# Optimization experiments

Measured on AMD Instinct MI355X. Metric: run time of the kernel, lower is better.

## Reference

```python
import jax, jax.numpy as jnp
import numpy as np

DIM = 256
NUM_HEADS = 8
HEAD_DIM = DIM // NUM_HEADS          # 32
KEY_DIM = int(HEAD_DIM * 0.5)        # 16
SCALE = KEY_DIM ** (-0.5)
QKV_OUT = DIM + 2 * KEY_DIM * NUM_HEADS  # 512
BN_EPS = 1e-3


def _bn(x, gamma, beta, mean, var):
    # inference-mode BatchNorm2d over channel axis 1 of NCHW
    inv = gamma / jnp.sqrt(var + BN_EPS)
    return x * inv[None, :, None, None] + (beta - mean * inv)[None, :, None, None]


def _conv1x1(x, w):
    # w: (O, C, 1, 1)
    return jnp.einsum('bchw,oc->bohw', x, w[:, :, 0, 0])


def _dwconv3x3(x, w):
    # depthwise 3x3, SAME padding; w: (C, 1, 3, 3)
    return jax.lax.conv_general_dilated(
        x, w, window_strides=(1, 1), padding='SAME',
        feature_group_count=x.shape[1],
        dimension_numbers=('NCHW', 'OIHW', 'NCHW'))


def setup_inputs() -> dict:
    key = jax.random.key(0)
    ks = jax.random.split(key, 16)
    B, C, H, W = 16, DIM, 32, 32
    inp = {
        'x': jax.random.normal(ks[0], (B, C, H, W), jnp.float32),
        'qkv_w': jax.random.normal(ks[1], (QKV_OUT, DIM, 1, 1), jnp.float32) * (1.0 / np.sqrt(DIM)),
        'qkv_gamma': jnp.ones((QKV_OUT,), jnp.float32),
        'qkv_beta': jnp.zeros((QKV_OUT,), jnp.float32),
        'qkv_mean': jax.random.normal(ks[2], (QKV_OUT,), jnp.float32) * 0.1,
        'qkv_var': jax.random.uniform(ks[3], (QKV_OUT,), jnp.float32, 0.5, 1.5),
        'pe_w': jax.random.normal(ks[4], (DIM, 1, 3, 3), jnp.float32) * (1.0 / 3.0),
        'pe_gamma': jnp.ones((DIM,), jnp.float32),
        'pe_beta': jnp.zeros((DIM,), jnp.float32),
        'pe_mean': jax.random.normal(ks[5], (DIM,), jnp.float32) * 0.1,
        'pe_var': jax.random.uniform(ks[6], (DIM,), jnp.float32, 0.5, 1.5),
        'proj_w': jax.random.normal(ks[7], (DIM, DIM, 1, 1), jnp.float32) * (1.0 / np.sqrt(DIM)),
        'proj_gamma': jnp.ones((DIM,), jnp.float32),
        'proj_beta': jnp.zeros((DIM,), jnp.float32),
        'proj_mean': jax.random.normal(ks[8], (DIM,), jnp.float32) * 0.1,
        'proj_var': jax.random.uniform(ks[9], (DIM,), jnp.float32, 0.5, 1.5),
    }
    return inp


def reference(x, qkv_w, qkv_gamma, qkv_beta, qkv_mean, qkv_var,
              pe_w, pe_gamma, pe_beta, pe_mean, pe_var,
              proj_w, proj_gamma, proj_beta, proj_mean, proj_var):
    B, C, H, W = x.shape
    N = H * W
    # qkv: 1x1 conv + BN (act=False)
    qkv = _bn(_conv1x1(x, qkv_w), qkv_gamma, qkv_beta, qkv_mean, qkv_var)
    qkv = qkv.reshape(B, NUM_HEADS, 2 * KEY_DIM + HEAD_DIM, N)
    q = qkv[:, :, :KEY_DIM]                          # (B, h, kd, N)
    k = qkv[:, :, KEY_DIM:2 * KEY_DIM]               # (B, h, kd, N)
    v = qkv[:, :, 2 * KEY_DIM:]                      # (B, h, hd, N)
    # attn = (q^T @ k) * scale, softmax over last dim
    attn = jnp.einsum('bhdn,bhdm->bhnm', q, k) * SCALE   # (B, h, N, N)
    attn = jax.nn.softmax(attn, axis=-1)
    # v @ attn^T
    v_attn = jnp.einsum('bhdn,bhmn->bhdm', v, attn)      # (B, h, hd, N)
    v_attn = v_attn.reshape(B, C, H, W)
    v_reshaped = v.reshape(B, C, H, W)
    pos_enc = _bn(_dwconv3x3(v_reshaped, pe_w), pe_gamma, pe_beta, pe_mean, pe_var)
    out = v_attn + pos_enc
    out = _bn(_conv1x1(out, proj_w), proj_gamma, proj_beta, proj_mean, proj_var)
    return out
```

## Files before the change

### kernel.cpp

```cpp
#include <hip/hip_runtime.h>

#define B_ 16
#define C_ 256
#define N_ 1024
#define NH 8
#define HD 32
#define KD 16
#define QKV_OUT_ 512
#define BN_EPS 1e-3f
#define SCALE_ 0.25f

typedef __attribute__((ext_vector_type(8))) short short8;
typedef __attribute__((ext_vector_type(16))) float float16;

__device__ inline unsigned short f2bf(float f) {
  unsigned int u = __float_as_uint(f);
  return (unsigned short)((u + 0x7FFF + ((u >> 16) & 1)) >> 16);
}
__device__ inline float bf2f(unsigned short s) {
  return __uint_as_float(((unsigned int)s) << 16);
}
__device__ inline float16 zero16() {
  float16 z;
  #pragma unroll
  for (int i = 0; i < 16; ++i) z[i] = 0.f;
  return z;
}
__device__ inline unsigned int pack_bf16_trunc(float a, float b) {
  return __builtin_amdgcn_perm(__float_as_uint(b), __float_as_uint(a), 0x07060302u);
}

__global__ __launch_bounds__(256) void fold_weights(
    const float* __restrict__ qkv_w, const float* __restrict__ qg,
    const float* __restrict__ qb, const float* __restrict__ qm,
    const float* __restrict__ qv,
    const float* __restrict__ proj_w, const float* __restrict__ pg,
    const float* __restrict__ pb, const float* __restrict__ pm,
    const float* __restrict__ pv,
    unsigned short* __restrict__ wq, float* __restrict__ biasq,
    unsigned short* __restrict__ wp, float* __restrict__ biasp)
{
  const int o = blockIdx.x, c = threadIdx.x;
  if (o < QKV_OUT_) {
    float inv = qg[o] * rsqrtf(qv[o] + BN_EPS);
    wq[o * C_ + c] = f2bf(qkv_w[o * C_ + c] * inv);
    if (c == 0) biasq[o] = qb[o] - qm[o] * inv;
  } else {
    int oo = o - QKV_OUT_;
    float inv = pg[oo] * rsqrtf(pv[oo] + BN_EPS);
    wp[oo * C_ + c] = f2bf(proj_w[oo * C_ + c] * inv);
    if (c == 0) biasp[oo] = pb[oo] - pm[oo] * inv;
  }
}

template <int OC, bool BF16OUT>
__global__ __launch_bounds__(256) void gemm_bn(
    const float* __restrict__ in, const unsigned short* __restrict__ wfold,
    const float* __restrict__ bias, void* __restrict__ out)
{
  __shared__ __align__(16) unsigned short xb[128][24];
  const int tid = threadIdx.x;
  const int wave = tid >> 6, lane = tid & 63, l31 = lane & 31, lh = lane >> 5;
  const int wm = wave & 1, wn = wave >> 1;
  const int nt = blockIdx.x, ot = blockIdx.y, b = blockIdx.z;

  const float* inb = in + (size_t)b * C_ * N_ + nt * 128;
  const int srow = tid & 127, sc0 = (tid >> 7) * 8;

  float16 acc0 = zero16(), acc1 = zero16();
  const unsigned short* wrow = wfold + (size_t)(ot * 64 + wm * 32 + l31) * C_;

  for (int kc = 0; kc < C_; kc += 16) {
    float xv[8];
    #pragma unroll
    for (int j = 0; j < 8; ++j)
      xv[j] = inb[(size_t)(kc + sc0 + j) * N_ + srow];
    unsigned int pk[4];
    #pragma unroll
    for (int q = 0; q < 4; ++q) pk[q] = pack_bf16_trunc(xv[2*q], xv[2*q+1]);
    __syncthreads();
    *(uint4*)&xb[srow][sc0] = make_uint4(pk[0], pk[1], pk[2], pk[3]);
    __syncthreads();

    short8 af = *(const short8*)(wrow + kc + lh * 8);
    short8 b0 = *(const short8*)&xb[wn * 64 + l31][lh * 8];
    short8 b1 = *(const short8*)&xb[wn * 64 + 32 + l31][lh * 8];
    acc0 = __builtin_amdgcn_mfma_f32_32x32x16_bf16(af, b0, acc0, 0, 0, 0);
    acc1 = __builtin_amdgcn_mfma_f32_32x32x16_bf16(af, b1, acc1, 0, 0, 0);
  }

  #pragma unroll
  for (int r = 0; r < 16; ++r) {
    int o = ot * 64 + wm * 32 + (r & 3) + 8 * (r >> 2) + 4 * lh;
    float bo = bias[o];
    size_t base = ((size_t)b * OC + o) * N_ + nt * 128 + wn * 64 + l31;
    float v0 = acc0[r] + bo, v1 = acc1[r] + bo;
    if constexpr (BF16OUT) {
      ((unsigned short*)out)[base]      = f2bf(v0);
      ((unsigned short*)out)[base + 32] = f2bf(v1);
    } else {
      ((float*)out)[base]      = v0;
      ((float*)out)[base + 32] = v1;
    }
  }
}

__global__ __launch_bounds__(256) void attn_mfma(
    const unsigned short* __restrict__ qkvb, float* __restrict__ vattn)
{
  const int wave = threadIdx.x >> 6, lane = threadIdx.x & 63;
  const int l31 = lane & 31, lh = lane >> 5;
  const int h = blockIdx.y, b = blockIdx.z;
  const int qbase = blockIdx.x * 128 + wave * 32;

  const unsigned short* qp = qkvb + ((size_t)b * QKV_OUT_ + h * 64) * N_;
  const unsigned short* kp = qp + (size_t)KD * N_;
  const unsigned short* vp = qp + (size_t)(2 * KD) * N_;

  short8 qf;
  #pragma unroll
  for (int j = 0; j < 8; ++j)
    qf[j] = (short)f2bf(bf2f(qp[(size_t)(lh * 8 + j) * N_ + qbase + l31]) * SCALE_);

  float16 oacc = zero16();
  float lsum = 0.f;

  for (int kc = 0; kc < N_; kc += 128) {
    #pragma unroll
    for (int t = 0; t < 4; ++t) {
      short8 kf;
      #pragma unroll
      for (int j = 0; j < 8; ++j)
        kf[j] = (short)kp[(size_t)(lh * 8 + j) * N_ + kc + t * 32 + l31];
      float16 st = __builtin_amdgcn_mfma_f32_32x32x16_bf16(kf, qf, zero16(), 0, 0, 0);

      unsigned int u[8];
      #pragma unroll
      for (int q = 0; q < 8; ++q) {
        float pe = __expf(st[2 * q]);
        float po = __expf(st[2 * q + 1]);
        lsum += pe + po;
        u[q] = pack_bf16_trunc(pe, po);
      }
      unsigned int e[8];
      #pragma unroll
      for (int q = 0; q < 8; ++q)
        e[q] = (unsigned int)__shfl_xor((int)u[q], 32, 64);

      #pragma unroll
      for (int f = 0; f < 2; ++f) {
        union { unsigned int w[4]; short8 s; } bf;
        int q0 = f * 4;
        bf.w[0] = lh ? e[q0 + 2] : u[q0 + 0];
        bf.w[1] = lh ? e[q0 + 3] : u[q0 + 1];
        bf.w[2] = lh ? u[q0 + 2] : e[q0 + 0];
        bf.w[3] = lh ? u[q0 + 3] : e[q0 + 1];
        short8 vf = *(const short8*)(vp + (size_t)l31 * N_ + kc + t * 32 + f * 16 + lh * 8);
        oacc = __builtin_amdgcn_mfma_f32_32x32x16_bf16(vf, bf.s, oacc, 0, 0, 0);
      }
    }
  }

  lsum += __shfl_xor(lsum, 32, 64);
  float linv = 1.f / lsum;

  #pragma unroll
  for (int r = 0; r < 16; ++r) {
    int d = (r & 3) + 8 * (r >> 2) + 4 * lh;
    vattn[((size_t)b * C_ + h * HD + d) * N_ + qbase + l31] = oacc[r] * linv;
  }
}

__global__ __launch_bounds__(256) void dwconv_bn_add(
    const unsigned short* __restrict__ qkvb, const float* __restrict__ pw,
    const float* __restrict__ gamma, const float* __restrict__ beta,
    const float* __restrict__ mean, const float* __restrict__ var,
    float* __restrict__ vsum)
{
  __shared__ float t[34][34];
  const int c = blockIdx.x, b = blockIdx.y;
  const int tid = threadIdx.x;
  const int qc = (c >> 5) * 64 + 32 + (c & 31);
  const unsigned short* vp = qkvb + ((size_t)b * QKV_OUT_ + qc) * N_;

  #pragma unroll
  for (int r = 0; r < 4; ++r) {
    int idx = r * 256 + tid;
    t[(idx >> 5) + 1][(idx & 31) + 1] = bf2f(vp[idx]);
  }
  if (tid < 34) {
    t[0][tid] = 0.f; t[33][tid] = 0.f;
    t[tid][0] = 0.f; t[tid][33] = 0.f;
  }
  __syncthreads();

  float w9[9];
  #pragma unroll
  for (int i = 0; i < 9; ++i) w9[i] = pw[c * 9 + i];
  float inv = gamma[c] * rsqrtf(var[c] + BN_EPS);
  float add = beta[c] - mean[c] * inv;

  float* op = vsum + ((size_t)b * C_ + c) * N_;
  #pragma unroll
  for (int r = 0; r < 4; ++r) {
    int idx = r * 256 + tid;
    int y = idx >> 5, x = idx & 31;
    float s = 0.f;
    #pragma unroll
    for (int dy = 0; dy < 3; ++dy)
      #pragma unroll
      for (int dx = 0; dx < 3; ++dx)
        s += t[y + dy][x + dx] * w9[dy * 3 + dx];
    op[idx] = s * inv + add + op[idx];
  }
}

extern "C" void kernel_launch(void* const* d_in, const int* in_sizes, int n_in,
                              void* d_out, int out_size, void* d_ws, size_t ws_size,
                              hipStream_t stream) {
  const float* x          = (const float*)d_in[0];
  const float* qkv_w      = (const float*)d_in[1];
  const float* qkv_gamma  = (const float*)d_in[2];
  const float* qkv_beta   = (const float*)d_in[3];
  const float* qkv_mean   = (const float*)d_in[4];
  const float* qkv_var    = (const float*)d_in[5];
  const float* pe_w       = (const float*)d_in[6];
  const float* pe_gamma   = (const float*)d_in[7];
  const float* pe_beta    = (const float*)d_in[8];
  const float* pe_mean    = (const float*)d_in[9];
  const float* pe_var     = (const float*)d_in[10];
  const float* proj_w     = (const float*)d_in[11];
  const float* proj_gamma = (const float*)d_in[12];
  const float* proj_beta  = (const float*)d_in[13];
  const float* proj_mean  = (const float*)d_in[14];
  const float* proj_var   = (const float*)d_in[15];
  float* out = (float*)d_out;

  char* ws = (char*)d_ws;
  unsigned short* qkvb = (unsigned short*)ws;
  ws += (size_t)B_ * QKV_OUT_ * N_ * sizeof(unsigned short);
  float* vattn = (float*)ws;
  ws += (size_t)B_ * C_ * N_ * sizeof(float);
  unsigned short* wq = (unsigned short*)ws;
  ws += (size_t)QKV_OUT_ * C_ * sizeof(unsigned short);
  unsigned short* wp = (unsigned short*)ws;
  ws += (size_t)C_ * C_ * sizeof(unsigned short);
  float* biasq = (float*)ws; ws += QKV_OUT_ * sizeof(float);
  float* biasp = (float*)ws;

  fold_weights<<<dim3(QKV_OUT_ + C_), 256, 0, stream>>>(
      qkv_w, qkv_gamma, qkv_beta, qkv_mean, qkv_var,
      proj_w, proj_gamma, proj_beta, proj_mean, proj_var,
      wq, biasq, wp, biasp);

  gemm_bn<QKV_OUT_, true><<<dim3(8, 8, 16), 256, 0, stream>>>(x, wq, biasq, qkvb);

  attn_mfma<<<dim3(8, NH, B_), 256, 0, stream>>>(qkvb, vattn);

  dwconv_bn_add<<<dim3(C_, B_), 256, 0, stream>>>(
      qkvb, pe_w, pe_gamma, pe_beta, pe_mean, pe_var, vattn);

  gemm_bn<C_, false><<<dim3(8, 4, 16), 256, 0, stream>>>(vattn, wp, biasp, out);
}
```

Measured before the change: 179.0 us.

## Transpose Q/K to token-major layout, double-buffer GEMM tiles, use exp2 softmax

```diff
diff --git a/kernel.cpp b/kernel.cpp
--- a/kernel.cpp
+++ b/kernel.cpp
@@ -8,7 +8,7 @@
 #define KD 16
 #define QKV_OUT_ 512
 #define BN_EPS 1e-3f
-#define SCALE_ 0.25f
+#define SCALE2_ (0.25f * 1.44269504088896f)
 
 typedef __attribute__((ext_vector_type(8))) short short8;
 typedef __attribute__((ext_vector_type(16))) float float16;
@@ -53,74 +53,131 @@
   }
 }
 
-template <int OC, bool BF16OUT>
+template <int MODE>
 __global__ __launch_bounds__(256) void gemm_bn(
     const float* __restrict__ in, const unsigned short* __restrict__ wfold,
-    const float* __restrict__ bias, void* __restrict__ out)
+    const float* __restrict__ bias,
+    unsigned short* __restrict__ qkT, unsigned short* __restrict__ vbuf,
+    float* __restrict__ outf)
 {
-  __shared__ __align__(16) unsigned short xb[128][24];
+  __shared__ __align__(16) unsigned short xb[2][256][20];
   const int tid = threadIdx.x;
   const int wave = tid >> 6, lane = tid & 63, l31 = lane & 31, lh = lane >> 5;
   const int wm = wave & 1, wn = wave >> 1;
   const int nt = blockIdx.x, ot = blockIdx.y, b = blockIdx.z;
 
-  const float* inb = in + (size_t)b * C_ * N_ + nt * 128;
-  const int srow = tid & 127, sc0 = (tid >> 7) * 8;
-
-  float16 acc0 = zero16(), acc1 = zero16();
+  const float* inb = in + (size_t)b * C_ * N_ + nt * 256 + tid;
   const unsigned short* wrow = wfold + (size_t)(ot * 64 + wm * 32 + l31) * C_;
 
-  for (int kc = 0; kc < C_; kc += 16) {
-    float xv[8];
-    #pragma unroll
-    for (int j = 0; j < 8; ++j)
-      xv[j] = inb[(size_t)(kc + sc0 + j) * N_ + srow];
-    unsigned int pk[4];
-    #pragma unroll
-    for (int q = 0; q < 4; ++q) pk[q] = pack_bf16_trunc(xv[2*q], xv[2*q+1]);
-    __syncthreads();
-    *(uint4*)&xb[srow][sc0] = make_uint4(pk[0], pk[1], pk[2], pk[3]);
-    __syncthreads();
-
-    short8 af = *(const short8*)(wrow + kc + lh * 8);
-    short8 b0 = *(const short8*)&xb[wn * 64 + l31][lh * 8];
-    short8 b1 = *(const short8*)&xb[wn * 64 + 32 + l31][lh * 8];
-    acc0 = __builtin_amdgcn_mfma_f32_32x32x16_bf16(af, b0, acc0, 0, 0, 0);
-    acc1 = __builtin_amdgcn_mfma_f32_32x32x16_bf16(af, b1, acc1, 0, 0, 0);
-  }
-
-  #pragma unroll
-  for (int r = 0; r < 16; ++r) {
-    int o = ot * 64 + wm * 32 + (r & 3) + 8 * (r >> 2) + 4 * lh;
-    float bo = bias[o];
-    size_t base = ((size_t)b * OC + o) * N_ + nt * 128 + wn * 64 + l31;
-    float v0 = acc0[r] + bo, v1 = acc1[r] + bo;
-    if constexpr (BF16OUT) {
-      ((unsigned short*)out)[base]      = f2bf(v0);
-      ((unsigned short*)out)[base + 32] = f2bf(v1);
+  float16 acc[4];
+  #pragma unroll
+  for (int i = 0; i < 4; ++i) acc[i] = zero16();
+
+  {
+    unsigned int pk[8];
+    #pragma unroll
+    for (int q = 0; q < 8; ++q) {
+      float a = inb[(size_t)(2 * q) * N_];
+      float c = inb[(size_t)(2 * q + 1) * N_];
+      pk[q] = pack_bf16_trunc(a, c);
+    }
+    #pragma unroll
+    for (int q = 0; q < 4; ++q)
+      *(uint2*)&xb[0][tid][q * 4] = make_uint2(pk[2 * q], pk[2 * q + 1]);
+  }
+  __syncthreads();
+
+  for (int s = 0; s < 16; ++s) {
+    const int buf = s & 1;
+    float nxt[16];
+    if (s < 15) {
+      #pragma unroll
+      for (int j = 0; j < 16; ++j)
+        nxt[j] = inb[(size_t)((s + 1) * 16 + j) * N_];
+    }
+
+    short8 a8 = *(const short8*)(wrow + s * 16 + lh * 8);
+    #pragma unroll
+    for (int sub = 0; sub < 4; ++sub) {
+      union { uint2 u[2]; short8 v; } bf;
+      const unsigned short* p = &xb[buf][wn * 128 + sub * 32 + l31][lh * 8];
+      bf.u[0] = *(const uint2*)p;
+      bf.u[1] = *(const uint2*)(p + 4);
+      acc[sub] = __builtin_amdgcn_mfma_f32_32x32x16_bf16(a8, bf.v, acc[sub], 0, 0, 0);
+    }
+
+    if (s < 15) {
+      unsigned int pk[8];
+      #pragma unroll
+      for (int q = 0; q < 8; ++q)
+        pk[q] = pack_bf16_trunc(nxt[2 * q], nxt[2 * q + 1]);
+      #pragma unroll
+      for (int q = 0; q < 4; ++q)
+        *(uint2*)&xb[buf ^ 1][tid][q * 4] = make_uint2(pk[2 * q], pk[2 * q + 1]);
+      __syncthreads();
+    }
+  }
+
+  if constexpr (MODE == 0) {
+    if (wm == 0) {
+      #pragma unroll
+      for (int sub = 0; sub < 4; ++sub) {
+        int token = nt * 256 + wn * 128 + sub * 32 + l31;
+        unsigned short* row = qkT + (((size_t)b * NH + ot) * N_ + token) * 32;
+        #pragma unroll
+        for (int qd = 0; qd < 4; ++qd) {
+          int cc0 = 8 * qd + 4 * lh;
+          ushort4 r;
+          r.x = f2bf(acc[sub][4 * qd + 0] + bias[ot * 64 + cc0 + 0]);
+          r.y = f2bf(acc[sub][4 * qd + 1] + bias[ot * 64 + cc0 + 1]);
+          r.z = f2bf(acc[sub][4 * qd + 2] + bias[ot * 64 + cc0 + 2]);
+          r.w = f2bf(acc[sub][4 * qd + 3] + bias[ot * 64 + cc0 + 3]);
+          *(ushort4*)(row + cc0) = r;
+        }
+      }
     } else {
-      ((float*)out)[base]      = v0;
-      ((float*)out)[base + 32] = v1;
+      #pragma unroll
+      for (int r = 0; r < 16; ++r) {
+        int cc = (r & 3) + 8 * (r >> 2) + 4 * lh;
+        float bo = bias[ot * 64 + 32 + cc];
+        unsigned short* vrow = vbuf + ((size_t)b * C_ + ot * 32 + cc) * N_ + nt * 256 + wn * 128 + l31;
+        #pragma unroll
+        for (int sub = 0; sub < 4; ++sub)
+          vrow[sub * 32] = f2bf(acc[sub][r] + bo);
+      }
+    }
+  } else {
+    #pragma unroll
+    for (int r = 0; r < 16; ++r) {
+      int o = ot * 64 + wm * 32 + (r & 3) + 8 * (r >> 2) + 4 * lh;
+      float bo = bias[o];
+      float* orow = outf + ((size_t)b * C_ + o) * N_ + nt * 256 + wn * 128 + l31;
+      #pragma unroll
+      for (int sub = 0; sub < 4; ++sub)
+        orow[sub * 32] = acc[sub][r] + bo;
     }
   }
 }
 
 __global__ __launch_bounds__(256) void attn_mfma(
-    const unsigned short* __restrict__ qkvb, float* __restrict__ vattn)
+    const unsigned short* __restrict__ qkT, const unsigned short* __restrict__ vbuf,
+    float* __restrict__ vattn)
 {
   const int wave = threadIdx.x >> 6, lane = threadIdx.x & 63;
   const int l31 = lane & 31, lh = lane >> 5;
   const int h = blockIdx.y, b = blockIdx.z;
   const int qbase = blockIdx.x * 128 + wave * 32;
 
-  const unsigned short* qp = qkvb + ((size_t)b * QKV_OUT_ + h * 64) * N_;
-  const unsigned short* kp = qp + (size_t)KD * N_;
-  const unsigned short* vp = qp + (size_t)(2 * KD) * N_;
+  const unsigned short* qkb = qkT + ((size_t)b * NH + h) * N_ * 32;
+  const unsigned short* vp = vbuf + ((size_t)b * C_ + h * HD + l31) * N_;
 
   short8 qf;
-  #pragma unroll
-  for (int j = 0; j < 8; ++j)
-    qf[j] = (short)f2bf(bf2f(qp[(size_t)(lh * 8 + j) * N_ + qbase + l31]) * SCALE_);
+  {
+    const unsigned short* qr = qkb + (size_t)(qbase + l31) * 32 + lh * 8;
+    #pragma unroll
+    for (int j = 0; j < 8; ++j)
+      qf[j] = (short)f2bf(bf2f(qr[j]) * SCALE2_);
+  }
 
   float16 oacc = zero16();
   float lsum = 0.f;
@@ -128,17 +185,15 @@
   for (int kc = 0; kc < N_; kc += 128) {
     #pragma unroll
     for (int t = 0; t < 4; ++t) {
-      short8 kf;
-      #pragma unroll
-      for (int j = 0; j < 8; ++j)
-        kf[j] = (short)kp[(size_t)(lh * 8 + j) * N_ + kc + t * 32 + l31];
+      int key0 = kc + t * 32;
+      short8 kf = *(const short8*)(qkb + (size_t)(key0 + l31) * 32 + 16 + lh * 8);
       float16 st = __builtin_amdgcn_mfma_f32_32x32x16_bf16(kf, qf, zero16(), 0, 0, 0);
 
       unsigned int u[8];
       #pragma unroll
       for (int q = 0; q < 8; ++q) {
-        float pe = __expf(st[2 * q]);
-        float po = __expf(st[2 * q + 1]);
+        float pe = exp2f(st[2 * q]);
+        float po = exp2f(st[2 * q + 1]);
         lsum += pe + po;
         u[q] = pack_bf16_trunc(pe, po);
       }
@@ -155,7 +210,7 @@
         bf.w[1] = lh ? e[q0 + 3] : u[q0 + 1];
         bf.w[2] = lh ? u[q0 + 2] : e[q0 + 0];
         bf.w[3] = lh ? u[q0 + 3] : e[q0 + 1];
-        short8 vf = *(const short8*)(vp + (size_t)l31 * N_ + kc + t * 32 + f * 16 + lh * 8);
+        short8 vf = *(const short8*)(vp + key0 + f * 16 + lh * 8);
         oacc = __builtin_amdgcn_mfma_f32_32x32x16_bf16(vf, bf.s, oacc, 0, 0, 0);
       }
     }
@@ -172,7 +227,7 @@
 }
 
 __global__ __launch_bounds__(256) void dwconv_bn_add(
-    const unsigned short* __restrict__ qkvb, const float* __restrict__ pw,
+    const unsigned short* __restrict__ vbuf, const float* __restrict__ pw,
     const float* __restrict__ gamma, const float* __restrict__ beta,
     const float* __restrict__ mean, const float* __restrict__ var,
     float* __restrict__ vsum)
@@ -180,8 +235,7 @@
   __shared__ float t[34][34];
   const int c = blockIdx.x, b = blockIdx.y;
   const int tid = threadIdx.x;
-  const int qc = (c >> 5) * 64 + 32 + (c & 31);
-  const unsigned short* vp = qkvb + ((size_t)b * QKV_OUT_ + qc) * N_;
+  const unsigned short* vp = vbuf + ((size_t)b * C_ + c) * N_;
 
   #pragma unroll
   for (int r = 0; r < 4; ++r) {
@@ -237,8 +291,10 @@
   float* out = (float*)d_out;
 
   char* ws = (char*)d_ws;
-  unsigned short* qkvb = (unsigned short*)ws;
-  ws += (size_t)B_ * QKV_OUT_ * N_ * sizeof(unsigned short);
+  unsigned short* qkT = (unsigned short*)ws;
+  ws += (size_t)B_ * NH * N_ * 32 * sizeof(unsigned short);
+  unsigned short* vbuf = (unsigned short*)ws;
+  ws += (size_t)B_ * C_ * N_ * sizeof(unsigned short);
   float* vattn = (float*)ws;
   ws += (size_t)B_ * C_ * N_ * sizeof(float);
   unsigned short* wq = (unsigned short*)ws;
@@ -253,12 +309,14 @@
       proj_w, proj_gamma, proj_beta, proj_mean, proj_var,
       wq, biasq, wp, biasp);
 
-  gemm_bn<QKV_OUT_, true><<<dim3(8, 8, 16), 256, 0, stream>>>(x, wq, biasq, qkvb);
-
-  attn_mfma<<<dim3(8, NH, B_), 256, 0, stream>>>(qkvb, vattn);
+  gemm_bn<0><<<dim3(4, 8, 16), 256, 0, stream>>>(
+      x, wq, biasq, qkT, vbuf, nullptr);
+
+  attn_mfma<<<dim3(8, NH, B_), 256, 0, stream>>>(qkT, vbuf, vattn);
 
   dwconv_bn_add<<<dim3(C_, B_), 256, 0, stream>>>(
-      qkvb, pe_w, pe_gamma, pe_beta, pe_mean, pe_var, vattn);
-
-  gemm_bn<C_, false><<<dim3(8, 4, 16), 256, 0, stream>>>(vattn, wp, biasp, out);
-}
+      vbuf, pe_w, pe_gamma, pe_beta, pe_mean, pe_var, vattn);
+
+  gemm_bn<1><<<dim3(4, 4, 16), 256, 0, stream>>>(
+      vattn, wp, biasp, nullptr, nullptr, out);
+}
```

New measurement: 185.6 us. 3.7% more time.
